# Optimization experiments

Measured on AMD Instinct MI355X. Metric: run time of the kernel, lower is better.

## Reference

```python
import jax, jax.numpy as jnp
import numpy as np

L, H, NH, PF = 2, 256, 8, 512
D = H // NH
SCALE = float(np.sqrt(D))  # transformerCPI scales by sqrt(hid_dim // n_heads)


def layernorm(x, g, b, eps=1e-5):
    m = x.mean(-1, keepdims=True)
    v = ((x - m) ** 2).mean(-1, keepdims=True)
    return (x - m) / jnp.sqrt(v + eps) * g + b


def mha(q, k, v, wq, bq, wk, bk, wv, bv, wo, bo):
    B, Tq, _ = q.shape
    Tk = k.shape[1]
    Q = (q @ wq + bq).reshape(B, Tq, NH, D).transpose(0, 2, 1, 3)  # [B,h,Tq,d]
    K = (k @ wk + bk).reshape(B, Tk, NH, D).transpose(0, 2, 1, 3)
    V = (v @ wv + bv).reshape(B, Tk, NH, D).transpose(0, 2, 1, 3)
    att = jax.nn.softmax(jnp.einsum('bhqd,bhkd->bhqk', Q, K) / SCALE, axis=-1)
    x = jnp.einsum('bhqk,bhkd->bhqd', att, V).transpose(0, 2, 1, 3).reshape(B, Tq, H)
    return x @ wo + bo, att


def setup_inputs() -> dict:
    key = jax.random.key(0)
    ks = iter(jax.random.split(key, 64))
    B, T, S, A = 16, 512, 1024, 64
    p = lambda shape: jax.random.normal(next(ks), shape, jnp.float32) * 0.02
    inp = {
        'trg': jax.random.normal(next(ks), (B, T, A), jnp.float32),
        'src': jax.random.normal(next(ks), (B, S, H), jnp.float32),
        'ft_w': p((A, H)), 'ft_b': jnp.zeros((H,), jnp.float32),
        'fc1_w': p((H, 256)), 'fc1_b': jnp.zeros((256,), jnp.float32),
        'fc2_w': p((256, 2)), 'fc2_b': jnp.zeros((2,), jnp.float32),
        'ln_g': jnp.ones((L, H), jnp.float32), 'ln_b': jnp.zeros((L, H), jnp.float32),
        'pf_w1': p((L, H, PF)), 'pf_b1': jnp.zeros((L, PF), jnp.float32),
        'pf_w2': p((L, PF, H)), 'pf_b2': jnp.zeros((L, H), jnp.float32),
    }
    for pre in ('sa', 'ea'):
        for nm in ('q', 'k', 'v', 'o'):
            inp[f'{pre}_w{nm}'] = p((L, H, H))
            inp[f'{pre}_b{nm}'] = jnp.zeros((L, H), jnp.float32)
    return inp


def reference(trg, src, ft_w, ft_b, sa_wq, sa_bq, sa_wk, sa_bk, sa_wv, sa_bv, sa_wo, sa_bo,
              ea_wq, ea_bq, ea_wk, ea_bk, ea_wv, ea_bv, ea_wo, ea_bo,
              pf_w1, pf_b1, pf_w2, pf_b2, ln_g, ln_b, fc1_w, fc1_b, fc2_w, fc2_b):
    x = trg @ ft_w + ft_b  # [B,T,H]
    att = None
    for l in range(L):  # small fixed layer count
        sa_out, _ = mha(x, x, x, sa_wq[l], sa_bq[l], sa_wk[l], sa_bk[l],
                        sa_wv[l], sa_bv[l], sa_wo[l], sa_bo[l])
        x = layernorm(x + sa_out, ln_g[l], ln_b[l])
        ea_out, att = mha(x, src, src, ea_wq[l], ea_bq[l], ea_wk[l], ea_bk[l],
                          ea_wv[l], ea_bv[l], ea_wo[l], ea_bo[l])
        x = layernorm(x + ea_out, ln_g[l], ln_b[l])
        ff = jax.nn.relu(x @ pf_w1[l] + pf_b1[l]) @ pf_w2[l] + pf_b2[l]
        x = layernorm(x + ff, ln_g[l], ln_b[l])
    # norm-based softmax pooling (vectorized form of the original double loop)
    w = jax.nn.softmax(jnp.linalg.norm(x, axis=2), axis=1)  # [B,T]
    pooled = jnp.einsum('bt,bth->bh', w, x)                 # [B,H]
    label = jax.nn.relu(pooled @ fc1_w + fc1_b) @ fc2_w + fc2_b  # [B,2]
    return label, pooled, att
```

## Files before the change

### kernel.cpp

```cpp
#include <hip/hip_runtime.h>


typedef __bf16 bfrag __attribute__((ext_vector_type(8)));
typedef float f32x4 __attribute__((ext_vector_type(4)));
typedef unsigned int uint4v __attribute__((ext_vector_type(4)));

__device__ __forceinline__ unsigned short f2bf(float x) {
  unsigned u = __float_as_uint(x);
  u += 0x7fff + ((u >> 16) & 1);
  return (unsigned short)(u >> 16);
}
__device__ __forceinline__ float bf2f(unsigned short h) {
  return __uint_as_float((unsigned)h << 16);
}
__device__ __forceinline__ void split2(float x, unsigned short& hi, unsigned short& lo) {
  hi = f2bf(x);
  lo = f2bf(x - bf2f(hi));
}

__device__ __forceinline__ void load16_lds(const short* g, short* l) {
  __builtin_amdgcn_global_load_lds(
      (const __attribute__((address_space(1))) unsigned int*)g,
      (__attribute__((address_space(3))) unsigned int*)l, 16, 0, 0);
}

struct WDesc { const float* src; long long dst; int K; int N; int tile0; int pad; };
struct WAll { WDesc d[21]; };

__global__ __launch_bounds__(256) void wsplit_all(
    WAll P, short* __restrict__ Th, short* __restrict__ Tl)
{
  __shared__ float t[32][33];
  const int bid = blockIdx.x;
  int i = 0;
  while (i < 20 && bid >= P.d[i + 1].tile0) i++;
  const float* __restrict__ W = P.d[i].src;
  const int K = P.d[i].K, N = P.d[i].N;
  const int lt = bid - P.d[i].tile0;
  const int ntn = N >> 5;
  const int n0 = (lt % ntn) * 32, k0 = (lt / ntn) * 32;
  short* th = Th + P.d[i].dst;
  short* tl = Tl + P.d[i].dst;
  const int tx = threadIdx.x & 31, ty = threadIdx.x >> 5;
#pragma unroll
  for (int p = 0; p < 4; p++)
    t[ty + p * 8][tx] = W[(size_t)(k0 + ty + p * 8) * N + n0 + tx];
  __syncthreads();
#pragma unroll
  for (int p = 0; p < 4; p++) {
    float v = t[tx][ty + p * 8];
    unsigned short hi, lo; split2(v, hi, lo);
    size_t o = (size_t)(n0 + ty + p * 8) * K + k0 + tx;
    th[o] = (short)hi; tl[o] = (short)lo;
  }
}

__global__ __launch_bounds__(256) void xsplit(
    const float* __restrict__ X, short* __restrict__ Xh, short* __restrict__ Xl,
    int n4)
{
  int i = blockIdx.x * 256 + threadIdx.x;
  if (i < n4) {
    float4 v = ((const float4*)X)[i];
    ushort4 h, l;
    split2(v.x, h.x, l.x); split2(v.y, h.y, l.y);
    split2(v.z, h.z, l.z); split2(v.w, h.w, l.w);
    ((ushort4*)Xh)[i] = h; ((ushort4*)Xl)[i] = l;
  }
}

#define GEMM128_CORE(Ah_g, Al_g, Bh_g, Bl_g, K)                                \
  for (int k0 = 0; k0 < K; k0 += 32) {                                         \
    _Pragma("unroll")                                                          \
    for (int i = 0; i < 2; i++) {                                              \
      const int row = i * 64 + w * 16 + srow;                                  \
      const size_t ga = (size_t)(m0 + row) * K + k0 + sc4 * 8;                 \
      const size_t gb = (size_t)(n0 + row) * K + k0 + sc4 * 8;                 \
      const int ldst = i * 2048 + w * 512;                                     \
      load16_lds(Ah_g + ga, &Asl[0][ldst]);                                    \
      load16_lds(Al_g + ga, &Asl[1][ldst]);                                    \
      load16_lds(Bh_g + gb, &Bsl[0][ldst]);                                    \
      load16_lds(Bl_g + gb, &Bsl[1][ldst]);                                    \
    }                                                                          \
    __syncthreads();                                                           \
    bfrag afh[4], afl[4], bfh[4], bfl[4];                                      \
    _Pragma("unroll")                                                          \
    for (int mi = 0; mi < 4; mi++) {                                           \
      const int r = wm * 64 + mi * 16 + l15;                                   \
      afh[mi] = *(const bfrag*)(&Asl[0][r * 32 + l4 * 8]);                     \
      afl[mi] = *(const bfrag*)(&Asl[1][r * 32 + l4 * 8]);                     \
    }                                                                          \
    _Pragma("unroll")                                                          \
    for (int ni = 0; ni < 4; ni++) {                                           \
      const int r = wn * 64 + ni * 16 + l15;                                   \
      bfh[ni] = *(const bfrag*)(&Bsl[0][r * 32 + l4 * 8]);                     \
      bfl[ni] = *(const bfrag*)(&Bsl[1][r * 32 + l4 * 8]);                     \
    }                                                                          \
    _Pragma("unroll")                                                          \
    for (int mi = 0; mi < 4; mi++)                                             \
      _Pragma("unroll")                                                        \
      for (int ni = 0; ni < 4; ni++) {                                         \
        acc[mi][ni] = __builtin_amdgcn_mfma_f32_16x16x32_bf16(afh[mi], bfh[ni], acc[mi][ni], 0, 0, 0); \
        acc[mi][ni] = __builtin_amdgcn_mfma_f32_16x16x32_bf16(afh[mi], bfl[ni], acc[mi][ni], 0, 0, 0); \
        acc[mi][ni] = __builtin_amdgcn_mfma_f32_16x16x32_bf16(afl[mi], bfh[ni], acc[mi][ni], 0, 0, 0); \
      }                                                                        \
    __syncthreads();                                                           \
  }

template <bool RELU, bool SPLIT, bool WRITE_C>
__global__ __launch_bounds__(256) void gemm_mfma(
    const short* __restrict__ Ah_g, const short* __restrict__ Al_g,
    const short* __restrict__ Bh_g, const short* __restrict__ Bl_g,
    const float* __restrict__ bias, float* __restrict__ C,
    short* __restrict__ Ch, short* __restrict__ Cl,
    int M, int N, int K)
{
  __shared__ short Asl[2][128 * 32];
  __shared__ short Bsl[2][128 * 32];
  const int tid = threadIdx.x;
  const int lane = tid & 63, w = tid >> 6;
  const int wm = w & 1, wn = w >> 1;
  const int m0 = blockIdx.x * 128, n0 = blockIdx.y * 128;
  const int srow = lane >> 2, sc4 = lane & 3;
  const int l15 = lane & 15, l4 = lane >> 4;
  f32x4 acc[4][4] = {};
  GEMM128_CORE(Ah_g, Al_g, Bh_g, Bl_g, K)
#pragma unroll
  for (int mi = 0; mi < 4; mi++)
#pragma unroll
    for (int ni = 0; ni < 4; ni++) {
      const int n = n0 + wn * 64 + ni * 16 + l15;
      const float bv = bias[n];
#pragma unroll
      for (int r = 0; r < 4; r++) {
        const int m = m0 + wm * 64 + mi * 16 + l4 * 4 + r;
        float v = acc[mi][ni][r] + bv;
        if (RELU) v = fmaxf(v, 0.f);
        const size_t o = (size_t)m * N + n;
        if constexpr (WRITE_C) C[o] = v;
        if constexpr (SPLIT) {
          unsigned short hh, ll; split2(v, hh, ll);
          Ch[o] = (short)hh; Cl[o] = (short)ll;
        }
      }
    }
}

__global__ __launch_bounds__(256) void gemm_qkv(
    const short* __restrict__ Ah_g, const short* __restrict__ Al_g,
    const short* __restrict__ Bh_g, const short* __restrict__ Bl_g,
    const float* __restrict__ b0, const float* __restrict__ b1,
    const float* __restrict__ b2,
    short* __restrict__ D0h, short* __restrict__ D0l,
    short* __restrict__ D1h, short* __restrict__ D1l,
    short* __restrict__ D2h, short* __restrict__ D2l,
    int M, int K, int tksh, int nseg)
{
  __shared__ short Asl[2][128 * 32];
  __shared__ short Bsl[2][128 * 32];
  const int tid = threadIdx.x;
  const int lane = tid & 63, w = tid >> 6;
  const int wm = w & 1, wn = w >> 1;
  const int m0 = blockIdx.x * 128, n0 = blockIdx.y * 128;
  const int srow = lane >> 2, sc4 = lane & 3;
  const int l15 = lane & 15, l4 = lane >> 4;
  f32x4 acc[4][4] = {};
  GEMM128_CORE(Ah_g, Al_g, Bh_g, Bl_g, K)
  const int seg = n0 >> 8;
  const bool vt = (seg == nseg - 1);
  const float* bias = (seg == 0) ? b0 : (seg == 1 ? b1 : b2);
  short* Ch = (seg == 0) ? D0h : (seg == 1 ? D1h : D2h);
  short* Cl = (seg == 0) ? D0l : (seg == 1 ? D1l : D2l);
#pragma unroll
  for (int mi = 0; mi < 4; mi++)
#pragma unroll
    for (int ni = 0; ni < 4; ni++) {
      const int n = n0 + wn * 64 + ni * 16 + l15;
      const int nl = n & 255;
      const float bv = bias[nl];
      if (vt) {
        const int m = m0 + wm * 64 + mi * 16 + l4 * 4;
        const int bb = m >> tksh, tt = m & ((1 << tksh) - 1);
        const size_t o = ((((size_t)bb * 8 + (nl >> 5)) * 32 + (nl & 31)) << tksh) + tt;
        unsigned long long wh = 0, wl = 0;
#pragma unroll
        for (int r = 0; r < 4; r++) {
          float v = acc[mi][ni][r] + bv;
          unsigned short hh, ll; split2(v, hh, ll);
          wh |= (unsigned long long)hh << (16 * r);
          wl |= (unsigned long long)ll << (16 * r);
        }
        *(unsigned long long*)(Ch + o) = wh;
        *(unsigned long long*)(Cl + o) = wl;
      } else {
#pragma unroll
        for (int r = 0; r < 4; r++) {
          const int m = m0 + wm * 64 + mi * 16 + l4 * 4 + r;
          float v = acc[mi][ni][r] + bv;
          unsigned short hh, ll; split2(v, hh, ll);
          const size_t o = (size_t)m * 256 + nl;
          Ch[o] = (short)hh; Cl[o] = (short)ll;
        }
      }
    }
}

template <int TK>
__global__ __launch_bounds__(512, 4) void attn_mfma(
    const short* __restrict__ Qh, const short* __restrict__ Ql,
    const short* __restrict__ Kh, const short* __restrict__ Kl,
    const short* __restrict__ Vth, const short* __restrict__ Vtl,
    short* __restrict__ Oh, short* __restrict__ Ol,
    float* __restrict__ att_out)
{
  __shared__ float sc[16 * TK];
  const int n = blockIdx.x;
  const int xcd = n & 7, ii = n >> 3;
  const int bh = xcd * 16 + (ii >> 5);
  const int q0 = (ii & 31) * 16;
  const int b = bh >> 3, h = bh & 7;
  const int tid = threadIdx.x;
  const int lane = tid & 63, w = tid >> 6;
  const int l15 = lane & 15, l4 = lane >> 4;
  const float inv_scale = 0.17677669529663687f;

  const size_t qbase = (((size_t)b * 512 + q0 + l15) * 8 + h) * 32 + l4 * 8;
  bfrag qh = *(const bfrag*)(Qh + qbase);
  bfrag ql = *(const bfrag*)(Ql + qbase);

#pragma unroll
  for (int t = 0; t < TK / 128; t++) {
    const int n0c = w * (TK / 8) + t * 16;
    const size_t kbase = (((size_t)b * TK + n0c + l15) * 8 + h) * 32 + l4 * 8;
    bfrag kh = *(const bfrag*)(Kh + kbase);
    bfrag kl = *(const bfrag*)(Kl + kbase);
    f32x4 acc = {};
    acc = __builtin_amdgcn_mfma_f32_16x16x32_bf16(qh, kh, acc, 0, 0, 0);
    acc = __builtin_amdgcn_mfma_f32_16x16x32_bf16(qh, kl, acc, 0, 0, 0);
    acc = __builtin_amdgcn_mfma_f32_16x16x32_bf16(ql, kh, acc, 0, 0, 0);
    const int col = n0c + l15;
#pragma unroll
    for (int r = 0; r < 4; r++) {
      const int row = l4 * 4 + r;
      sc[row * TK + ((((col >> 2) ^ (row & 7)) << 2) | (col & 3))] = acc[r] * inv_scale;
    }
  }
  __syncthreads();

  const int sr = tid >> 5, sj = tid & 31, srsw = sr & 7;
  float mx = -1e30f;
  for (int k = sj; k < TK; k += 32)
    mx = fmaxf(mx, sc[sr * TK + ((((k >> 2) ^ srsw) << 2) | (k & 3))]);
#pragma unroll
  for (int off = 16; off > 0; off >>= 1) mx = fmaxf(mx, __shfl_xor(mx, off, 32));
  float sum = 0.f;
  for (int k = sj; k < TK; k += 32) {
    const int idx = sr * TK + ((((k >> 2) ^ srsw) << 2) | (k & 3));
    float e = __expf(sc[idx] - mx);
    sc[idx] = e;
    sum += e;
  }
#pragma unroll
  for (int off = 16; off > 0; off >>= 1) sum += __shfl_xor(sum, off, 32);
  const float inv = 1.f / sum;
  __syncthreads();

  if (att_out) {
    const size_t orow = (((size_t)(b * 8 + h)) * 512 + q0 + sr) * TK;
#pragma unroll
    for (int t = 0; t < TK / 128; t++) {
      const int g = sj + 32 * t;
      float4 e4 = *(const float4*)&sc[sr * TK + ((g ^ srsw) << 2)];
      e4.x *= inv; e4.y *= inv; e4.z *= inv; e4.w *= inv;
      *(float4*)&att_out[orow + g * 4] = e4;
    }
  }

  f32x4 oa0 = {}, oa1 = {};
  const float* pr = sc + l15 * TK;
  const int psw = l15 & 7;
  const size_t vb0 = (((size_t)(b * 8 + h)) * 32 + l15) * TK;
#pragma unroll
  for (int kc = w * (TK / 8); kc < (w + 1) * (TK / 8); kc += 32) {
    const int g0 = (kc >> 2) + l4 * 2;
    float4 p0 = *(const float4*)(pr + ((g0 ^ psw) << 2));
    float4 p1 = *(const float4*)(pr + (((g0 + 1) ^ psw) << 2));
    float f[8] = {p0.x, p0.y, p0.z, p0.w, p1.x, p1.y, p1.z, p1.w};
    uint4v uh, ul;
#pragma unroll
    for (int i = 0; i < 4; i++) {
      unsigned short h0, l0, h1, l1;
      split2(f[2 * i], h0, l0); split2(f[2 * i + 1], h1, l1);
      uh[i] = (unsigned)h0 | ((unsigned)h1 << 16);
      ul[i] = (unsigned)l0 | ((unsigned)l1 << 16);
    }
    bfrag ph = __builtin_bit_cast(bfrag, uh);
    bfrag pl = __builtin_bit_cast(bfrag, ul);
    const size_t vk = vb0 + kc + l4 * 8;
    bfrag v0h = *(const bfrag*)(Vth + vk);
    bfrag v0l = *(const bfrag*)(Vtl + vk);
    bfrag v1h = *(const bfrag*)(Vth + vk + (size_t)16 * TK);
    bfrag v1l = *(const bfrag*)(Vtl + vk + (size_t)16 * TK);
    oa0 = __builtin_amdgcn_mfma_f32_16x16x32_bf16(ph, v0h, oa0, 0, 0, 0);
    oa0 = __builtin_amdgcn_mfma_f32_16x16x32_bf16(ph, v0l, oa0, 0, 0, 0);
    oa0 = __builtin_amdgcn_mfma_f32_16x16x32_bf16(pl, v0h, oa0, 0, 0, 0);
    oa1 = __builtin_amdgcn_mfma_f32_16x16x32_bf16(ph, v1h, oa1, 0, 0, 0);
    oa1 = __builtin_amdgcn_mfma_f32_16x16x32_bf16(ph, v1l, oa1, 0, 0, 0);
    oa1 = __builtin_amdgcn_mfma_f32_16x16x32_bf16(pl, v1h, oa1, 0, 0, 0);
  }
  __syncthreads();
  float* obuf = sc;
#pragma unroll
  for (int r = 0; r < 4; r++) {
    obuf[(w * 16 + l4 * 4 + r) * 33 + l15]      = oa0[r];
    obuf[(w * 16 + l4 * 4 + r) * 33 + 16 + l15] = oa1[r];
  }
  __syncthreads();
  {
    float s0 = 0.f;
#pragma unroll
    for (int ww = 0; ww < 8; ww++)
      s0 += obuf[(ww * 16 + sr) * 33 + sj];
    s0 *= inv;
    unsigned short h0, l0;
    split2(s0, h0, l0);
    const size_t ob = (((size_t)b * 512 + q0 + sr) * 8 + h) * 32 + sj;
    Oh[ob] = (short)h0;  Ol[ob] = (short)l0;
  }
}

template <bool WNORM>
__global__ __launch_bounds__(256) void residual_ln(
    float* __restrict__ x, const float* __restrict__ sub,
    const float* __restrict__ g, const float* __restrict__ bi,
    short* __restrict__ xh, short* __restrict__ xl, float* __restrict__ nrm)
{
  const int wid = threadIdx.x >> 6, lane = threadIdx.x & 63;
  const size_t row = (size_t)blockIdx.x * 4 + wid;
  const int c = lane * 4;
  float4 xv = *(const float4*)&x[row * 256 + c];
  float4 sv = *(const float4*)&sub[row * 256 + c];
  float v0 = xv.x + sv.x, v1 = xv.y + sv.y, v2 = xv.z + sv.z, v3 = xv.w + sv.w;
  float s = v0 + v1 + v2 + v3;
#pragma unroll
  for (int off = 32; off > 0; off >>= 1) s += __shfl_xor(s, off, 64);
  const float mean = s * (1.f / 256.f);
  const float d0 = v0 - mean, d1 = v1 - mean, d2 = v2 - mean, d3 = v3 - mean;
  float s2 = d0 * d0 + d1 * d1 + d2 * d2 + d3 * d3;
#pragma unroll
  for (int off = 32; off > 0; off >>= 1) s2 += __shfl_xor(s2, off, 64);
  const float rs = rsqrtf(s2 * (1.f / 256.f) + 1e-5f);
  const float4 gv = *(const float4*)&g[c];
  const float4 bv = *(const float4*)&bi[c];
  const float y0 = d0 * rs * gv.x + bv.x, y1 = d1 * rs * gv.y + bv.y;
  const float y2 = d2 * rs * gv.z + bv.z, y3 = d3 * rs * gv.w + bv.w;
  float4 yo; yo.x = y0; yo.y = y1; yo.z = y2; yo.w = y3;
  *(float4*)&x[row * 256 + c] = yo;
  ushort4 hh, ll;
  split2(y0, hh.x, ll.x); split2(y1, hh.y, ll.y);
  split2(y2, hh.z, ll.z); split2(y3, hh.w, ll.w);
  *(ushort4*)&xh[row * 256 + c] = hh;
  *(ushort4*)&xl[row * 256 + c] = ll;
  if (WNORM) {
    float ns = y0 * y0 + y1 * y1 + y2 * y2 + y3 * y3;
#pragma unroll
    for (int off = 32; off > 0; off >>= 1) ns += __shfl_xor(ns, off, 64);
    if (lane == 0) nrm[row] = sqrtf(ns);
  }
}

__global__ __launch_bounds__(256) void pool1(
    const float* __restrict__ x, const float* __restrict__ nrm,
    float* __restrict__ partial)
{
  __shared__ float w[512];
  __shared__ float red[4];
  const int b = blockIdx.x, cchunk = blockIdx.y, tid = threadIdx.x;
  float n0 = nrm[b * 512 + tid], n1 = nrm[b * 512 + 256 + tid];
  float lm = fmaxf(n0, n1);
  for (int off = 32; off > 0; off >>= 1) lm = fmaxf(lm, __shfl_xor(lm, off, 64));
  if ((tid & 63) == 0) red[tid >> 6] = lm;
  __syncthreads();
  float m = fmaxf(fmaxf(red[0], red[1]), fmaxf(red[2], red[3]));
  float e0 = __expf(n0 - m), e1 = __expf(n1 - m);
  float ls = e0 + e1;
  for (int off = 32; off > 0; off >>= 1) ls += __shfl_xor(ls, off, 64);
  __syncthreads();
  if ((tid & 63) == 0) red[tid >> 6] = ls;
  __syncthreads();
  float inv = 1.f / (red[0] + red[1] + red[2] + red[3]);
  w[tid] = e0 * inv; w[tid + 256] = e1 * inv;
  __syncthreads();
  float acc = 0.f;
  const int t0 = cchunk * 128;
  for (int t = t0; t < t0 + 128; t++)
    acc += w[t] * x[((size_t)b * 512 + t) * 256 + tid];
  partial[((size_t)b * 4 + cchunk) * 256 + tid] = acc;
}

__global__ __launch_bounds__(256) void pool2(
    const float* __restrict__ partial, float* __restrict__ pooled,
    float* __restrict__ pooled_out)
{
  const int b = blockIdx.x, tid = threadIdx.x;
  float s = partial[((size_t)b * 4 + 0) * 256 + tid]
          + partial[((size_t)b * 4 + 1) * 256 + tid]
          + partial[((size_t)b * 4 + 2) * 256 + tid]
          + partial[((size_t)b * 4 + 3) * 256 + tid];
  pooled[b * 256 + tid] = s;
  pooled_out[b * 256 + tid] = s;
}

__global__ __launch_bounds__(256) void fc_head(
    const float* __restrict__ pooled,
    const float* __restrict__ fc1_w, const float* __restrict__ fc1_b,
    const float* __restrict__ fc2_w, const float* __restrict__ fc2_b,
    float* __restrict__ label_out)
{
  __shared__ float pl[256];
  __shared__ float hid[256];
  const int b = blockIdx.x, tid = threadIdx.x;
  pl[tid] = pooled[b * 256 + tid];
  __syncthreads();
  float acc = fc1_b[tid];
  for (int k = 0; k < 256; k++)
    acc += pl[k] * fc1_w[k * 256 + tid];
  hid[tid] = fmaxf(acc, 0.f);
  __syncthreads();
  if (tid < 2) {
    float s = fc2_b[tid];
    for (int k = 0; k < 256; k++)
      s += hid[k] * fc2_w[k * 2 + tid];
    label_out[b * 2 + tid] = s;
  }
}

extern "C" void kernel_launch(void* const* d_in, const int* in_sizes, int n_in,
                              void* d_out, int out_size, void* d_ws, size_t ws_size,
                              hipStream_t stream)
{
  const float* trg   = (const float*)d_in[0];
  const float* src   = (const float*)d_in[1];
  const float* ft_w  = (const float*)d_in[2];
  const float* ft_b  = (const float*)d_in[3];
  const float* fc1_w = (const float*)d_in[4];
  const float* fc1_b = (const float*)d_in[5];
  const float* fc2_w = (const float*)d_in[6];
  const float* fc2_b = (const float*)d_in[7];
  const float* ln_g  = (const float*)d_in[8];
  const float* ln_b  = (const float*)d_in[9];
  const float* pf_w1 = (const float*)d_in[10];
  const float* pf_b1 = (const float*)d_in[11];
  const float* pf_w2 = (const float*)d_in[12];
  const float* pf_b2 = (const float*)d_in[13];
  const float* aw[2][8];
  for (int p = 0; p < 2; p++)
    for (int i = 0; i < 8; i++) aw[p][i] = (const float*)d_in[14 + p * 8 + i];
  float* outp = (float*)d_out;

  char* wsb = (char*)d_ws;
  const size_t MB = 1u << 20;
  float* x    = (float*)(wsb);
  float* sub  = (float*)(wsb + 8 * MB);
  short* x_hi = (short*)(wsb + 16 * MB);
  short* x_lo = (short*)(wsb + 20 * MB);
  short* qbh  = (short*)(wsb + 24 * MB);
  short* qbl  = (short*)(wsb + 28 * MB);
  short* kbh  = (short*)(wsb + 32 * MB);
  short* kbl  = (short*)(wsb + 40 * MB);
  short* vth  = (short*)(wsb + 48 * MB);
  short* vtl  = (short*)(wsb + 56 * MB);
  short* obh  = (short*)(wsb + 64 * MB);
  short* obl  = (short*)(wsb + 68 * MB);
  short* srch = (short*)(wsb + 72 * MB);
  short* srcl = (short*)(wsb + 80 * MB);
  short* w_hi = (short*)(wsb + 88 * MB);
  short* w_lo = (short*)(wsb + 92 * MB);
  short* ffmh = kbh;
  short* ffml = kbl;
  short* trgh = vth;
  short* trgl = vtl;
  float* nrm  = (float*)qbh;
  float* pld  = (float*)qbh + 8192;
  float* part = (float*)qbh + 16384;

  auto woff = [](int l, int idx) -> size_t {
    size_t base = 16384 + (size_t)l * 786432;
    if (idx < 8)  return base + (size_t)idx * 65536;
    if (idx == 8) return base + 524288;
    return base + 655360;
  };

  {
    WAll P{};
    int t = 0, e = 0;
    auto add = [&](const float* s, int K, int N, size_t dst) {
      P.d[e].src = s; P.d[e].dst = (long long)dst;
      P.d[e].K = K; P.d[e].N = N; P.d[e].tile0 = t;
      t += (K / 32) * (N / 32); e++;
    };
    add(ft_w, 64, 256, 0);
    for (int l = 0; l < 2; l++) {
      const size_t wo = (size_t)l * 65536;
      for (int i = 0; i < 4; i++) add(aw[0][2 * i] + wo, 256, 256, woff(l, i));
      for (int i = 0; i < 4; i++) add(aw[1][2 * i] + wo, 256, 256, woff(l, 4 + i));
      add(pf_w1 + (size_t)l * 131072, 256, 512, woff(l, 8));
      add(pf_w2 + (size_t)l * 131072, 512, 256, woff(l, 9));
    }
    wsplit_all<<<t, 256, 0, stream>>>(P, w_hi, w_lo);
  }
  xsplit<<<512, 256, 0, stream>>>(trg, trgh, trgl, 131072);
  xsplit<<<4096, 256, 0, stream>>>(src, srch, srcl, 1048576);

  gemm_mfma<false, true, true><<<dim3(64, 2), 256, 0, stream>>>(
      trgh, trgl, w_hi, w_lo, ft_b, x, x_hi, x_lo, 8192, 256, 64);

  for (int l = 0; l < 2; l++) {
    const size_t bo = (size_t)l * 256;
    gemm_qkv<<<dim3(64, 6), 256, 0, stream>>>(
        x_hi, x_lo, w_hi + woff(l, 0), w_lo + woff(l, 0),
        aw[0][1] + bo, aw[0][3] + bo, aw[0][5] + bo,
        qbh, qbl, kbh, kbl, vth, vtl, 8192, 256, 9, 3);
    attn_mfma<512><<<4096, 512, 0, stream>>>(
        qbh, qbl, kbh, kbl, vth, vtl, obh, obl, (float*)nullptr);
    gemm_mfma<false, false, true><<<dim3(64, 2), 256, 0, stream>>>(
        obh, obl, w_hi + woff(l, 3), w_lo + woff(l, 3), aw[0][7] + bo,
        sub, nullptr, nullptr, 8192, 256, 256);
    residual_ln<false><<<2048, 256, 0, stream>>>(x, sub, ln_g + bo, ln_b + bo,
                                                 x_hi, x_lo, nullptr);
    gemm_mfma<false, true, false><<<dim3(64, 2), 256, 0, stream>>>(
        x_hi, x_lo, w_hi + woff(l, 4), w_lo + woff(l, 4), aw[1][1] + bo,
        nullptr, qbh, qbl, 8192, 256, 256);
    gemm_qkv<<<dim3(128, 4), 256, 0, stream>>>(
        srch, srcl, w_hi + woff(l, 5), w_lo + woff(l, 5),
        aw[1][3] + bo, aw[1][5] + bo, nullptr,
        kbh, kbl, vth, vtl, nullptr, nullptr, 16384, 256, 10, 2);
    {
      float* att = (l == 1) ? (outp + 4128) : (float*)nullptr;
      attn_mfma<1024><<<4096, 512, 0, stream>>>(
          qbh, qbl, kbh, kbl, vth, vtl, obh, obl, att);
    }
    gemm_mfma<false, false, true><<<dim3(64, 2), 256, 0, stream>>>(
        obh, obl, w_hi + woff(l, 7), w_lo + woff(l, 7), aw[1][7] + bo,
        sub, nullptr, nullptr, 8192, 256, 256);
    residual_ln<false><<<2048, 256, 0, stream>>>(x, sub, ln_g + bo, ln_b + bo,
                                                 x_hi, x_lo, nullptr);
    gemm_mfma<true, true, false><<<dim3(64, 4), 256, 0, stream>>>(
        x_hi, x_lo, w_hi + woff(l, 8), w_lo + woff(l, 8), pf_b1 + (size_t)l * 512,
        nullptr, ffmh, ffml, 8192, 512, 256);
    gemm_mfma<false, false, true><<<dim3(64, 2), 256, 0, stream>>>(
        ffmh, ffml, w_hi + woff(l, 9), w_lo + woff(l, 9), pf_b2 + bo,
        sub, nullptr, nullptr, 8192, 256, 512);
    if (l == 0) {
      residual_ln<false><<<2048, 256, 0, stream>>>(x, sub, ln_g + bo, ln_b + bo,
                                                   x_hi, x_lo, nullptr);
    } else {
      residual_ln<true><<<2048, 256, 0, stream>>>(x, sub, ln_g + bo, ln_b + bo,
                                                  x_hi, x_lo, nrm);
    }
  }

  pool1<<<dim3(16, 4), 256, 0, stream>>>(x, nrm, part);
  pool2<<<16, 256, 0, stream>>>(part, pld, outp + 32);
  fc_head<<<16, 256, 0, stream>>>(pld, fc1_w, fc1_b, fc2_w, fc2_b, outp);
}
```

Measured before the change: 1.068 ms.

## Fuse output GEMMs with residual layernorm and batch encoder K/V projections

Adds a gemm_oln kernel that computes the full 256-wide row output of the O-projection and FFN2 GEMMs and applies bias, residual add and layernorm in its epilogue. This removes the separate residual_ln pass and the fp32 sub buffer round trip. Both layers' encoder-attention K/V projections of src are hoisted into one up-front gemm_eakv launch with separate buffers, and pool2/fc_head are merged. The trade-off is that gemm_oln runs only 128 blocks of 64 rows with a single-buffered, unpipelined K loop, which may underfill the GPU compared with the 128-block 2D grids it replaces.

```diff
diff --git a/kernel.cpp b/kernel.cpp
--- a/kernel.cpp
+++ b/kernel.cpp
@@ -154,7 +154,7 @@
     short* __restrict__ D0h, short* __restrict__ D0l,
     short* __restrict__ D1h, short* __restrict__ D1l,
     short* __restrict__ D2h, short* __restrict__ D2l,
-    int M, int K, int tksh, int nseg)
+    int M, int K, int tksh)
 {
   __shared__ short Asl[2][128 * 32];
   __shared__ short Bsl[2][128 * 32];
@@ -167,7 +167,7 @@
   f32x4 acc[4][4] = {};
   GEMM128_CORE(Ah_g, Al_g, Bh_g, Bl_g, K)
   const int seg = n0 >> 8;
-  const bool vt = (seg == nseg - 1);
+  const bool vt = (seg == 2);
   const float* bias = (seg == 0) ? b0 : (seg == 1 ? b1 : b2);
   short* Ch = (seg == 0) ? D0h : (seg == 1 ? D1h : D2h);
   short* Cl = (seg == 0) ? D0l : (seg == 1 ? D1l : D2l);
@@ -203,6 +203,223 @@
         }
       }
     }
+}
+
+__global__ __launch_bounds__(256) void gemm_eakv(
+    const short* __restrict__ Ah_g, const short* __restrict__ Al_g,
+    const short* __restrict__ Bh_g, const short* __restrict__ Bl_g,
+    const float* __restrict__ bk0, const float* __restrict__ bv0,
+    const float* __restrict__ bk1, const float* __restrict__ bv1,
+    short* __restrict__ K0h, short* __restrict__ K0l,
+    short* __restrict__ V0h, short* __restrict__ V0l,
+    short* __restrict__ K1h, short* __restrict__ K1l,
+    short* __restrict__ V1h, short* __restrict__ V1l,
+    int M, int K)
+{
+  __shared__ short Asl[2][128 * 32];
+  __shared__ short Bsl[2][128 * 32];
+  const int tid = threadIdx.x;
+  const int lane = tid & 63, w = tid >> 6;
+  const int wm = w & 1, wn = w >> 1;
+  const int m0 = blockIdx.x * 128, n0 = blockIdx.y * 128;
+  const int srow = lane >> 2, sc4 = lane & 3;
+  const int l15 = lane & 15, l4 = lane >> 4;
+  f32x4 acc[4][4] = {};
+  GEMM128_CORE(Ah_g, Al_g, Bh_g, Bl_g, K)
+  const int seg = n0 >> 8;
+  const bool vt = (seg & 1);
+  const float* bias = (seg == 0) ? bk0 : (seg == 1 ? bv0 : (seg == 2 ? bk1 : bv1));
+  short* Ch = (seg == 0) ? K0h : (seg == 1 ? V0h : (seg == 2 ? K1h : V1h));
+  short* Cl = (seg == 0) ? K0l : (seg == 1 ? V0l : (seg == 2 ? K1l : V1l));
+#pragma unroll
+  for (int mi = 0; mi < 4; mi++)
+#pragma unroll
+    for (int ni = 0; ni < 4; ni++) {
+      const int n = n0 + wn * 64 + ni * 16 + l15;
+      const int nl = n & 255;
+      const float bv = bias[nl];
+      if (vt) {
+        const int m = m0 + wm * 64 + mi * 16 + l4 * 4;
+        const int bb = m >> 10, tt = m & 1023;
+        const size_t o = ((((size_t)bb * 8 + (nl >> 5)) * 32 + (nl & 31)) << 10) + tt;
+        unsigned long long wh = 0, wl = 0;
+#pragma unroll
+        for (int r = 0; r < 4; r++) {
+          float v = acc[mi][ni][r] + bv;
+          unsigned short hh, ll; split2(v, hh, ll);
+          wh |= (unsigned long long)hh << (16 * r);
+          wl |= (unsigned long long)ll << (16 * r);
+        }
+        *(unsigned long long*)(Ch + o) = wh;
+        *(unsigned long long*)(Cl + o) = wl;
+      } else {
+#pragma unroll
+        for (int r = 0; r < 4; r++) {
+          const int m = m0 + wm * 64 + mi * 16 + l4 * 4 + r;
+          float v = acc[mi][ni][r] + bv;
+          unsigned short hh, ll; split2(v, hh, ll);
+          const size_t o = (size_t)m * 256 + nl;
+          Ch[o] = (short)hh; Cl[o] = (short)ll;
+        }
+      }
+    }
+}
+
+template <bool WNORM>
+__global__ __launch_bounds__(256) void gemm_oln(
+    const short* __restrict__ Ah_g, const short* __restrict__ Al_g,
+    const short* __restrict__ Bh_g, const short* __restrict__ Bl_g,
+    const float* __restrict__ bias, const float* __restrict__ g,
+    const float* __restrict__ bi, float* __restrict__ x,
+    short* __restrict__ xh, short* __restrict__ xl,
+    float* __restrict__ nrm, int K)
+{
+  __shared__ short Asl[2][64 * 32];
+  __shared__ short Bsl[2][256 * 32];
+  __shared__ float red[512];
+  const int tid = threadIdx.x;
+  const int lane = tid & 63, w = tid >> 6;
+  const int m0 = blockIdx.x * 64;
+  const int l15 = lane & 15, l4 = lane >> 4;
+  f32x4 acc[4][4] = {};
+
+  for (int k0 = 0; k0 < K; k0 += 32) {
+    {
+      const int arow = tid >> 2, ac4 = tid & 3;
+      const size_t ga = (size_t)(m0 + arow) * K + k0 + ac4 * 8;
+      load16_lds(Ah_g + ga, &Asl[0][w * 512]);
+      load16_lds(Al_g + ga, &Asl[1][w * 512]);
+#pragma unroll
+      for (int i = 0; i < 4; i++) {
+        const int c = i * 256 + tid;
+        const int brow = c >> 2, bc4 = c & 3;
+        const size_t gb = (size_t)brow * K + k0 + bc4 * 8;
+        load16_lds(Bh_g + gb, &Bsl[0][i * 2048 + w * 512]);
+        load16_lds(Bl_g + gb, &Bsl[1][i * 2048 + w * 512]);
+      }
+    }
+    __syncthreads();
+    bfrag afh[4], afl[4], bfh[4], bfl[4];
+#pragma unroll
+    for (int mi = 0; mi < 4; mi++) {
+      const int r = mi * 16 + l15;
+      afh[mi] = *(const bfrag*)(&Asl[0][r * 32 + l4 * 8]);
+      afl[mi] = *(const bfrag*)(&Asl[1][r * 32 + l4 * 8]);
+    }
+#pragma unroll
+    for (int ni = 0; ni < 4; ni++) {
+      const int c = w * 64 + ni * 16 + l15;
+      bfh[ni] = *(const bfrag*)(&Bsl[0][c * 32 + l4 * 8]);
+      bfl[ni] = *(const bfrag*)(&Bsl[1][c * 32 + l4 * 8]);
+    }
+#pragma unroll
+    for (int mi = 0; mi < 4; mi++)
+#pragma unroll
+      for (int ni = 0; ni < 4; ni++) {
+        acc[mi][ni] = __builtin_amdgcn_mfma_f32_16x16x32_bf16(afh[mi], bfh[ni], acc[mi][ni], 0, 0, 0);
+        acc[mi][ni] = __builtin_amdgcn_mfma_f32_16x16x32_bf16(afh[mi], bfl[ni], acc[mi][ni], 0, 0, 0);
+        acc[mi][ni] = __builtin_amdgcn_mfma_f32_16x16x32_bf16(afl[mi], bfh[ni], acc[mi][ni], 0, 0, 0);
+      }
+    __syncthreads();
+  }
+  float biasv[4], gv[4], bvv[4];
+#pragma unroll
+  for (int ni = 0; ni < 4; ni++) {
+    const int col = w * 64 + ni * 16 + l15;
+    biasv[ni] = bias[col]; gv[ni] = g[col]; bvv[ni] = bi[col];
+  }
+#pragma unroll
+  for (int mi = 0; mi < 4; mi++)
+#pragma unroll
+    for (int r = 0; r < 4; r++) {
+      const size_t row = m0 + mi * 16 + l4 * 4 + r;
+#pragma unroll
+      for (int ni = 0; ni < 4; ni++)
+        acc[mi][ni][r] += biasv[ni] + x[row * 256 + w * 64 + ni * 16 + l15];
+    }
+#pragma unroll
+  for (int mi = 0; mi < 4; mi++)
+#pragma unroll
+    for (int r = 0; r < 4; r++) {
+      float s = acc[mi][0][r] + acc[mi][1][r] + acc[mi][2][r] + acc[mi][3][r];
+#pragma unroll
+      for (int off = 1; off < 16; off <<= 1) s += __shfl_xor(s, off, 16);
+      if (l15 == 0) red[(mi * 16 + l4 * 4 + r) * 4 + w] = s;
+    }
+  __syncthreads();
+  float mean[4][4];
+#pragma unroll
+  for (int mi = 0; mi < 4; mi++)
+#pragma unroll
+    for (int r = 0; r < 4; r++) {
+      const int lr = mi * 16 + l4 * 4 + r;
+      mean[mi][r] = (red[lr * 4] + red[lr * 4 + 1] + red[lr * 4 + 2] + red[lr * 4 + 3]) * (1.f / 256.f);
+    }
+  __syncthreads();
+#pragma unroll
+  for (int mi = 0; mi < 4; mi++)
+#pragma unroll
+    for (int r = 0; r < 4; r++) {
+      float s2 = 0.f;
+#pragma unroll
+      for (int ni = 0; ni < 4; ni++) {
+        const float d = acc[mi][ni][r] - mean[mi][r];
+        s2 += d * d;
+      }
+#pragma unroll
+      for (int off = 1; off < 16; off <<= 1) s2 += __shfl_xor(s2, off, 16);
+      if (l15 == 0) red[(mi * 16 + l4 * 4 + r) * 4 + w] = s2;
+    }
+  __syncthreads();
+  float rs[4][4];
+#pragma unroll
+  for (int mi = 0; mi < 4; mi++)
+#pragma unroll
+    for (int r = 0; r < 4; r++) {
+      const int lr = mi * 16 + l4 * 4 + r;
+      const float var = (red[lr * 4] + red[lr * 4 + 1] + red[lr * 4 + 2] + red[lr * 4 + 3]) * (1.f / 256.f);
+      rs[mi][r] = rsqrtf(var + 1e-5f);
+    }
+  if (WNORM) __syncthreads();
+  float wn2[4][4];
+#pragma unroll
+  for (int mi = 0; mi < 4; mi++)
+#pragma unroll
+    for (int r = 0; r < 4; r++) {
+      wn2[mi][r] = 0.f;
+      const size_t row = m0 + mi * 16 + l4 * 4 + r;
+#pragma unroll
+      for (int ni = 0; ni < 4; ni++) {
+        const int col = w * 64 + ni * 16 + l15;
+        const float y = (acc[mi][ni][r] - mean[mi][r]) * rs[mi][r] * gv[ni] + bvv[ni];
+        x[row * 256 + col] = y;
+        unsigned short hh, ll; split2(y, hh, ll);
+        xh[row * 256 + col] = (short)hh;
+        xl[row * 256 + col] = (short)ll;
+        if (WNORM) wn2[mi][r] += y * y;
+      }
+    }
+  if (WNORM) {
+#pragma unroll
+    for (int mi = 0; mi < 4; mi++)
+#pragma unroll
+      for (int r = 0; r < 4; r++) {
+        float s2 = wn2[mi][r];
+#pragma unroll
+        for (int off = 1; off < 16; off <<= 1) s2 += __shfl_xor(s2, off, 16);
+        if (l15 == 0) red[(mi * 16 + l4 * 4 + r) * 4 + w] = s2;
+      }
+    __syncthreads();
+    if (w == 0 && l15 == 0) {
+#pragma unroll
+      for (int mi = 0; mi < 4; mi++)
+#pragma unroll
+        for (int r = 0; r < 4; r++) {
+          const int lr = mi * 16 + l4 * 4 + r;
+          nrm[m0 + lr] = sqrtf(red[lr * 4] + red[lr * 4 + 1] + red[lr * 4 + 2] + red[lr * 4 + 3]);
+        }
+    }
+  }
 }
 
 template <int TK>
@@ -329,46 +546,6 @@
   }
 }
 
-template <bool WNORM>
-__global__ __launch_bounds__(256) void residual_ln(
-    float* __restrict__ x, const float* __restrict__ sub,
-    const float* __restrict__ g, const float* __restrict__ bi,
-    short* __restrict__ xh, short* __restrict__ xl, float* __restrict__ nrm)
-{
-  const int wid = threadIdx.x >> 6, lane = threadIdx.x & 63;
-  const size_t row = (size_t)blockIdx.x * 4 + wid;
-  const int c = lane * 4;
-  float4 xv = *(const float4*)&x[row * 256 + c];
-  float4 sv = *(const float4*)&sub[row * 256 + c];
-  float v0 = xv.x + sv.x, v1 = xv.y + sv.y, v2 = xv.z + sv.z, v3 = xv.w + sv.w;
-  float s = v0 + v1 + v2 + v3;
-#pragma unroll
-  for (int off = 32; off > 0; off >>= 1) s += __shfl_xor(s, off, 64);
-  const float mean = s * (1.f / 256.f);
-  const float d0 = v0 - mean, d1 = v1 - mean, d2 = v2 - mean, d3 = v3 - mean;
-  float s2 = d0 * d0 + d1 * d1 + d2 * d2 + d3 * d3;
-#pragma unroll
-  for (int off = 32; off > 0; off >>= 1) s2 += __shfl_xor(s2, off, 64);
-  const float rs = rsqrtf(s2 * (1.f / 256.f) + 1e-5f);
-  const float4 gv = *(const float4*)&g[c];
-  const float4 bv = *(const float4*)&bi[c];
-  const float y0 = d0 * rs * gv.x + bv.x, y1 = d1 * rs * gv.y + bv.y;
-  const float y2 = d2 * rs * gv.z + bv.z, y3 = d3 * rs * gv.w + bv.w;
-  float4 yo; yo.x = y0; yo.y = y1; yo.z = y2; yo.w = y3;
-  *(float4*)&x[row * 256 + c] = yo;
-  ushort4 hh, ll;
-  split2(y0, hh.x, ll.x); split2(y1, hh.y, ll.y);
-  split2(y2, hh.z, ll.z); split2(y3, hh.w, ll.w);
-  *(ushort4*)&xh[row * 256 + c] = hh;
-  *(ushort4*)&xl[row * 256 + c] = ll;
-  if (WNORM) {
-    float ns = y0 * y0 + y1 * y1 + y2 * y2 + y3 * y3;
-#pragma unroll
-    for (int off = 32; off > 0; off >>= 1) ns += __shfl_xor(ns, off, 64);
-    if (lane == 0) nrm[row] = sqrtf(ns);
-  }
-}
-
 __global__ __launch_bounds__(256) void pool1(
     const float* __restrict__ x, const float* __restrict__ nrm,
     float* __restrict__ partial)
@@ -398,29 +575,21 @@
   partial[((size_t)b * 4 + cchunk) * 256 + tid] = acc;
 }
 
-__global__ __launch_bounds__(256) void pool2(
-    const float* __restrict__ partial, float* __restrict__ pooled,
-    float* __restrict__ pooled_out)
-{
+__global__ __launch_bounds__(256) void pool2fc(
+    const float* __restrict__ partial, float* __restrict__ pooled_out,
+    const float* __restrict__ fc1_w, const float* __restrict__ fc1_b,
+    const float* __restrict__ fc2_w, const float* __restrict__ fc2_b,
+    float* __restrict__ label_out)
+{
+  __shared__ float pl[256];
+  __shared__ float hid[256];
   const int b = blockIdx.x, tid = threadIdx.x;
   float s = partial[((size_t)b * 4 + 0) * 256 + tid]
           + partial[((size_t)b * 4 + 1) * 256 + tid]
           + partial[((size_t)b * 4 + 2) * 256 + tid]
           + partial[((size_t)b * 4 + 3) * 256 + tid];
-  pooled[b * 256 + tid] = s;
   pooled_out[b * 256 + tid] = s;
-}
-
-__global__ __launch_bounds__(256) void fc_head(
-    const float* __restrict__ pooled,
-    const float* __restrict__ fc1_w, const float* __restrict__ fc1_b,
-    const float* __restrict__ fc2_w, const float* __restrict__ fc2_b,
-    float* __restrict__ label_out)
-{
-  __shared__ float pl[256];
-  __shared__ float hid[256];
-  const int b = blockIdx.x, tid = threadIdx.x;
-  pl[tid] = pooled[b * 256 + tid];
+  pl[tid] = s;
   __syncthreads();
   float acc = fc1_b[tid];
   for (int k = 0; k < 256; k++)
@@ -428,10 +597,10 @@
   hid[tid] = fmaxf(acc, 0.f);
   __syncthreads();
   if (tid < 2) {
-    float s = fc2_b[tid];
+    float s2 = fc2_b[tid];
     for (int k = 0; k < 256; k++)
-      s += hid[k] * fc2_w[k * 2 + tid];
-    label_out[b * 2 + tid] = s;
+      s2 += hid[k] * fc2_w[k * 2 + tid];
+    label_out[b * 2 + tid] = s2;
   }
 }
 
@@ -460,36 +629,33 @@
 
   char* wsb = (char*)d_ws;
   const size_t MB = 1u << 20;
-  float* x    = (float*)(wsb);
-  float* sub  = (float*)(wsb + 8 * MB);
-  short* x_hi = (short*)(wsb + 16 * MB);
-  short* x_lo = (short*)(wsb + 20 * MB);
-  short* qbh  = (short*)(wsb + 24 * MB);
-  short* qbl  = (short*)(wsb + 28 * MB);
-  short* kbh  = (short*)(wsb + 32 * MB);
-  short* kbl  = (short*)(wsb + 40 * MB);
-  short* vth  = (short*)(wsb + 48 * MB);
-  short* vtl  = (short*)(wsb + 56 * MB);
-  short* obh  = (short*)(wsb + 64 * MB);
-  short* obl  = (short*)(wsb + 68 * MB);
-  short* srch = (short*)(wsb + 72 * MB);
-  short* srcl = (short*)(wsb + 80 * MB);
-  short* w_hi = (short*)(wsb + 88 * MB);
-  short* w_lo = (short*)(wsb + 92 * MB);
-  short* ffmh = kbh;
-  short* ffml = kbl;
-  short* trgh = vth;
-  short* trgl = vtl;
+  float* x     = (float*)(wsb);
+  short* x_hi  = (short*)(wsb + 8 * MB);
+  short* x_lo  = (short*)(wsb + 12 * MB);
+  short* qbh   = (short*)(wsb + 16 * MB);
+  short* qbl   = (short*)(wsb + 20 * MB);
+  short* sakh  = (short*)(wsb + 24 * MB);
+  short* sakl  = (short*)(wsb + 28 * MB);
+  short* savth = (short*)(wsb + 32 * MB);
+  short* savtl = (short*)(wsb + 36 * MB);
+  short* obh   = (short*)(wsb + 40 * MB);
+  short* obl   = (short*)(wsb + 44 * MB);
+  short* srch  = (short*)(wsb + 48 * MB);
+  short* srcl  = (short*)(wsb + 56 * MB);
+  short* eakh[2]  = {(short*)(wsb + 64 * MB),  (short*)(wsb + 96 * MB)};
+  short* eakl[2]  = {(short*)(wsb + 72 * MB),  (short*)(wsb + 104 * MB)};
+  short* eavth[2] = {(short*)(wsb + 80 * MB),  (short*)(wsb + 112 * MB)};
+  short* eavtl[2] = {(short*)(wsb + 88 * MB),  (short*)(wsb + 120 * MB)};
+  short* ffmh  = (short*)(wsb + 128 * MB);
+  short* ffml  = (short*)(wsb + 136 * MB);
+  short* w_hi  = (short*)(wsb + 144 * MB);
+  short* w_lo  = (short*)(wsb + 148 * MB);
+  short* trgh = ffmh;
+  short* trgl = ffml;
   float* nrm  = (float*)qbh;
-  float* pld  = (float*)qbh + 8192;
-  float* part = (float*)qbh + 16384;
-
-  auto woff = [](int l, int idx) -> size_t {
-    size_t base = 16384 + (size_t)l * 786432;
-    if (idx < 8)  return base + (size_t)idx * 65536;
-    if (idx == 8) return base + 524288;
-    return base + 655360;
-  };
+  float* part = (float*)qbh + 8192;
+
+  auto Lb = [](int l) -> size_t { return 278528 + (size_t)l * 655360; };
 
   {
     WAll P{};
@@ -500,17 +666,31 @@
       t += (K / 32) * (N / 32); e++;
     };
     add(ft_w, 64, 256, 0);
+    add(aw[1][2], 256, 256, 16384);
+    add(aw[1][4], 256, 256, 81920);
+    add(aw[1][2] + 65536, 256, 256, 147456);
+    add(aw[1][4] + 65536, 256, 256, 212992);
     for (int l = 0; l < 2; l++) {
       const size_t wo = (size_t)l * 65536;
-      for (int i = 0; i < 4; i++) add(aw[0][2 * i] + wo, 256, 256, woff(l, i));
-      for (int i = 0; i < 4; i++) add(aw[1][2 * i] + wo, 256, 256, woff(l, 4 + i));
-      add(pf_w1 + (size_t)l * 131072, 256, 512, woff(l, 8));
-      add(pf_w2 + (size_t)l * 131072, 512, 256, woff(l, 9));
+      add(aw[0][0] + wo, 256, 256, Lb(l));
+      add(aw[0][2] + wo, 256, 256, Lb(l) + 65536);
+      add(aw[0][4] + wo, 256, 256, Lb(l) + 131072);
+      add(aw[0][6] + wo, 256, 256, Lb(l) + 196608);
+      add(aw[1][0] + wo, 256, 256, Lb(l) + 262144);
+      add(aw[1][6] + wo, 256, 256, Lb(l) + 327680);
+      add(pf_w1 + (size_t)l * 131072, 256, 512, Lb(l) + 393216);
+      add(pf_w2 + (size_t)l * 131072, 512, 256, Lb(l) + 524288);
     }
     wsplit_all<<<t, 256, 0, stream>>>(P, w_hi, w_lo);
   }
   xsplit<<<512, 256, 0, stream>>>(trg, trgh, trgl, 131072);
   xsplit<<<4096, 256, 0, stream>>>(src, srch, srcl, 1048576);
+
+  gemm_eakv<<<dim3(128, 8), 256, 0, stream>>>(
+      srch, srcl, w_hi + 16384, w_lo + 16384,
+      aw[1][3], aw[1][5], aw[1][3] + 256, aw[1][5] + 256,
+      eakh[0], eakl[0], eavth[0], eavtl[0],
+      eakh[1], eakl[1], eavth[1], eavtl[1], 16384, 256);
 
   gemm_mfma<false, true, true><<<dim3(64, 2), 256, 0, stream>>>(
       trgh, trgl, w_hi, w_lo, ft_b, x, x_hi, x_lo, 8192, 256, 64);
@@ -518,49 +698,40 @@
   for (int l = 0; l < 2; l++) {
     const size_t bo = (size_t)l * 256;
     gemm_qkv<<<dim3(64, 6), 256, 0, stream>>>(
-        x_hi, x_lo, w_hi + woff(l, 0), w_lo + woff(l, 0),
+        x_hi, x_lo, w_hi + Lb(l), w_lo + Lb(l),
         aw[0][1] + bo, aw[0][3] + bo, aw[0][5] + bo,
-        qbh, qbl, kbh, kbl, vth, vtl, 8192, 256, 9, 3);
+        qbh, qbl, sakh, sakl, savth, savtl, 8192, 256, 9);
     attn_mfma<512><<<4096, 512, 0, stream>>>(
-        qbh, qbl, kbh, kbl, vth, vtl, obh, obl, (float*)nullptr);
-    gemm_mfma<false, false, true><<<dim3(64, 2), 256, 0, stream>>>(
-        obh, obl, w_hi + woff(l, 3), w_lo + woff(l, 3), aw[0][7] + bo,
-        sub, nullptr, nullptr, 8192, 256, 256);
-    residual_ln<false><<<2048, 256, 0, stream>>>(x, sub, ln_g + bo, ln_b + bo,
-                                                 x_hi, x_lo, nullptr);
+        qbh, qbl, sakh, sakl, savth, savtl, obh, obl, (float*)nullptr);
+    gemm_oln<false><<<128, 256, 0, stream>>>(
+        obh, obl, w_hi + Lb(l) + 196608, w_lo + Lb(l) + 196608,
+        aw[0][7] + bo, ln_g + bo, ln_b + bo, x, x_hi, x_lo, nullptr, 256);
     gemm_mfma<false, true, false><<<dim3(64, 2), 256, 0, stream>>>(
-        x_hi, x_lo, w_hi + woff(l, 4), w_lo + woff(l, 4), aw[1][1] + bo,
-        nullptr, qbh, qbl, 8192, 256, 256);
-    gemm_qkv<<<dim3(128, 4), 256, 0, stream>>>(
-        srch, srcl, w_hi + woff(l, 5), w_lo + woff(l, 5),
-        aw[1][3] + bo, aw[1][5] + bo, nullptr,
-        kbh, kbl, vth, vtl, nullptr, nullptr, 16384, 256, 10, 2);
+        x_hi, x_lo, w_hi + Lb(l) + 262144, w_lo + Lb(l) + 262144,
+        aw[1][1] + bo, nullptr, qbh, qbl, 8192, 256, 256);
     {
       float* att = (l == 1) ? (outp + 4128) : (float*)nullptr;
       attn_mfma<1024><<<4096, 512, 0, stream>>>(
-          qbh, qbl, kbh, kbl, vth, vtl, obh, obl, att);
-    }
-    gemm_mfma<false, false, true><<<dim3(64, 2), 256, 0, stream>>>(
-        obh, obl, w_hi + woff(l, 7), w_lo + woff(l, 7), aw[1][7] + bo,
-        sub, nullptr, nullptr, 8192, 256, 256);
-    residual_ln<false><<<2048, 256, 0, stream>>>(x, sub, ln_g + bo, ln_b + bo,
-                                                 x_hi, x_lo, nullptr);
+          qbh, qbl, eakh[l], eakl[l], eavth[l], eavtl[l], obh, obl, att);
+    }
+    gemm_oln<false><<<128, 256, 0, stream>>>(
+        obh, obl, w_hi + Lb(l) + 327680, w_lo + Lb(l) + 327680,
+        aw[1][7] + bo, ln_g + bo, ln_b + bo, x, x_hi, x_lo, nullptr, 256);
     gemm_mfma<true, true, false><<<dim3(64, 4), 256, 0, stream>>>(
-        x_hi, x_lo, w_hi + woff(l, 8), w_lo + woff(l, 8), pf_b1 + (size_t)l * 512,
-        nullptr, ffmh, ffml, 8192, 512, 256);
-    gemm_mfma<false, false, true><<<dim3(64, 2), 256, 0, stream>>>(
-        ffmh, ffml, w_hi + woff(l, 9), w_lo + woff(l, 9), pf_b2 + bo,
-        sub, nullptr, nullptr, 8192, 256, 512);
+        x_hi, x_lo, w_hi + Lb(l) + 393216, w_lo + Lb(l) + 393216,
+        pf_b1 + (size_t)l * 512, nullptr, ffmh, ffml, 8192, 512, 256);
     if (l == 0) {
-      residual_ln<false><<<2048, 256, 0, stream>>>(x, sub, ln_g + bo, ln_b + bo,
-                                                   x_hi, x_lo, nullptr);
+      gemm_oln<false><<<128, 256, 0, stream>>>(
+          ffmh, ffml, w_hi + Lb(l) + 524288, w_lo + Lb(l) + 524288,
+          pf_b2 + bo, ln_g + bo, ln_b + bo, x, x_hi, x_lo, nullptr, 512);
     } else {
-      residual_ln<true><<<2048, 256, 0, stream>>>(x, sub, ln_g + bo, ln_b + bo,
-                                                  x_hi, x_lo, nrm);
+      gemm_oln<true><<<128, 256, 0, stream>>>(
+          ffmh, ffml, w_hi + Lb(l) + 524288, w_lo + Lb(l) + 524288,
+          pf_b2 + bo, ln_g + bo, ln_b + bo, x, x_hi, x_lo, nrm, 512);
     }
   }
 
   pool1<<<dim3(16, 4), 256, 0, stream>>>(x, nrm, part);
-  pool2<<<16, 256, 0, stream>>>(part, pld, outp + 32);
-  fc_head<<<16, 256, 0, stream>>>(pld, fc1_w, fc1_b, fc2_w, fc2_b, outp);
-}
+  pool2fc<<<16, 256, 0, stream>>>(part, outp + 32, fc1_w, fc1_b,
+                                  fc2_w, fc2_b, outp);
+}
```

Result: slower. 1.121 ms (+4.9%).
